# Performance work log

Measured on AMD Instinct MI355X. Metric: run time of the kernel, lower is better.

## Reference

```python
import jax, jax.numpy as jnp
import numpy as np
import math

D_MODEL = 1024
EXPAND = 2
D_INNER = D_MODEL * EXPAND  # 2048
D_STATE = 16
DT_RANK = max(1, (D_MODEL + 15) // 16)  # 64
K = 4  # conv kernel size
B, S = 2, 2048


def silu(v):
    return v * jax.nn.sigmoid(v)


def setup_inputs() -> dict:
    key = jax.random.key(0)
    ks = jax.random.split(key, 12)
    sc = lambda fan_in: 1.0 / math.sqrt(fan_in)
    x = jax.random.normal(ks[0], (B, S, D_MODEL), dtype=jnp.float32)
    Win = jax.random.normal(ks[1], (D_MODEL, 2 * D_INNER), dtype=jnp.float32) * sc(D_MODEL)
    Wconv = jax.random.normal(ks[2], (D_INNER, 1, K), dtype=jnp.float32) * sc(K)
    bconv = jax.random.normal(ks[3], (D_INNER,), dtype=jnp.float32) * 0.01
    Wx = jax.random.normal(ks[4], (D_INNER, DT_RANK + 2 * D_STATE), dtype=jnp.float32) * sc(D_INNER)
    Wdt = jax.random.normal(ks[5], (DT_RANK, D_INNER), dtype=jnp.float32) * sc(DT_RANK)
    # dt_proj bias init: inverse-softplus of dt ~ LogUniform[1e-3, 1e-1]
    dt = jnp.exp(jax.random.uniform(ks[6], (D_INNER,)) * (math.log(0.1) - math.log(0.001)) + math.log(0.001))
    dt = jnp.clip(dt, 0.0001, None)
    bdt = dt + jnp.log(-jnp.expm1(-dt))
    a = jnp.arange(1, D_STATE + 1, dtype=jnp.float32)[None, :].repeat(D_INNER, axis=0)
    a = a + jax.random.uniform(ks[7], a.shape) * 0.1
    A_log = jnp.log(a)
    Dp = jnp.ones((D_INNER,), dtype=jnp.float32)
    Wout = jax.random.normal(ks[8], (D_INNER, D_MODEL), dtype=jnp.float32) * sc(D_INNER)
    return {"x": x, "Win": Win, "Wconv": Wconv, "bconv": bconv, "Wx": Wx,
            "Wdt": Wdt, "bdt": bdt, "A_log": A_log, "Dp": Dp, "Wout": Wout}


def causal_dw_conv(x, Wconv, bconv):
    # x: [B, S, C] -> depthwise causal conv along S
    xc = jnp.transpose(x, (0, 2, 1))  # [B, C, S]
    y = jax.lax.conv_general_dilated(
        xc, Wconv, window_strides=(1,), padding=[(K - 1, 0)],
        feature_group_count=D_INNER,
        dimension_numbers=("NCH", "OIH", "NCH"))
    y = y + bconv[None, :, None]
    return jnp.transpose(y, (0, 2, 1))  # [B, S, C]


def selective_scan(u, delta, b_term, c_term, A_log, Dp):
    # u, delta: [B,S,Di]; b_term, c_term: [B,S,Ds]
    a = -jnp.exp(A_log)  # [Di, Ds]
    delta_a = jnp.exp(delta[..., None] * a[None, None])            # [B,S,Di,Ds] fp32
    delta_b_u = (delta * u)[..., None] * b_term[:, :, None, :]     # [B,S,Di,Ds]
    du = u * Dp[None, None, :]                                     # [B,S,Di]
    # time-major for scan
    dA = jnp.transpose(delta_a, (1, 0, 2, 3))
    dBu = jnp.transpose(delta_b_u, (1, 0, 2, 3))
    c_t = jnp.transpose(c_term, (1, 0, 2))
    du_t = jnp.transpose(du, (1, 0, 2))

    def step(state, inp):
        dA_t, dBu_t, c, duv = inp
        state = dA_t * state + dBu_t                  # [B,Di,Ds]
        y = jnp.einsum("bdn,bn->bd", state, c) + duv  # [B,Di]
        return state, y

    init = jnp.zeros((u.shape[0], D_INNER, D_STATE), dtype=jnp.float32)
    _, ys = jax.lax.scan(step, init, (dA, dBu, c_t, du_t))
    return jnp.transpose(ys, (1, 0, 2))  # [B,S,Di]


def reference(x, Win, Wconv, bconv, Wx, Wdt, bdt, A_log, Dp, Wout):
    xz = x @ Win                              # [B,S,2*Di]
    x_branch, z_branch = jnp.split(xz, 2, axis=-1)
    x_branch = silu(causal_dw_conv(x_branch, Wconv, bconv))
    params = x_branch @ Wx                    # [B,S,R+2*Ds]
    delta, b_term, c_term = jnp.split(params, [DT_RANK, DT_RANK + D_STATE], axis=-1)
    delta = jax.nn.softplus(delta @ Wdt + bdt)
    y = selective_scan(x_branch, delta, b_term, c_term, A_log, Dp)
    y = y * silu(z_branch)
    return y @ Wout
```

## Files before the change

### kernel.cpp

```cpp
#include <hip/hip_runtime.h>

typedef unsigned short u16;
typedef _Float16 f16;
typedef f16 f16x8 __attribute__((ext_vector_type(8)));
typedef u16 u16x8 __attribute__((ext_vector_type(8)));
typedef short s16x8 __attribute__((ext_vector_type(8)));
typedef float f32x4 __attribute__((ext_vector_type(4)));
typedef float f32x8 __attribute__((ext_vector_type(8)));

#define T_TOK 4096
#define B_SZ 2
#define S_LEN 2048
#define DMODEL 1024
#define DI 2048
#define DS 16
#define RNK 64
#define NCH 64
#define CLEN 32
#define LDXZ 4096
#define SK 8
#define PRM_SLICE (4096 * 128)
#define LOG2E 1.4426950408889634f

#define GLOAD_LDS16(gp, lp)                                                                   \
  __builtin_amdgcn_global_load_lds((const __attribute__((address_space(1))) void*)(gp),       \
                                   (__attribute__((address_space(3))) void*)(lp), 16, 0, 0)

__device__ __forceinline__ float b2f(u16 v) { return __uint_as_float(((unsigned)v) << 16); }
__device__ __forceinline__ u16 f2b(float f) {
  unsigned u = __float_as_uint(f);
  return (u16)((u + 0x7fffu + ((u >> 16) & 1u)) >> 16);
}
__device__ __forceinline__ float fexp2(float x) {
#if __has_builtin(__builtin_amdgcn_exp2f)
  return __builtin_amdgcn_exp2f(x);
#else
  return exp2f(x);
#endif
}
__device__ __forceinline__ int dtype_of(const void* dp) {
  unsigned v = *(const unsigned*)dp;
  return (v == 0x3F800000u) ? 0 : (v == 0x3C003C00u) ? 2 : 1;
}
__device__ __forceinline__ float load_any(const void* p, size_t i, int flag) {
  if (flag == 0) return ((const float*)p)[i];
  if (flag == 1) return b2f(((const u16*)p)[i]);
  return (float)((const f16*)p)[i];
}

__device__ __forceinline__ void tr_tile(const void* __restrict__ src, void* __restrict__ dst,
                                        int R, int C, int Cpad, int f, int bx, int by, int ob) {
  __shared__ f16 t[32][33];
  int c0 = bx * 32, r0 = by * 32;
  int tx = threadIdx.x & 31, ty = threadIdx.x >> 5;
#pragma unroll
  for (int i = ty; i < 32; i += 8) {
    int r = r0 + i, c = c0 + tx;
    float v = (r < R && c < C) ? load_any(src, (size_t)r * C + c, f) : 0.f;
    t[i][tx] = (f16)v;
  }
  __syncthreads();
#pragma unroll
  for (int i = ty; i < 32; i += 8) {
    int c = c0 + i, r = r0 + tx;
    if (c < Cpad && r < R) {
      if (ob) ((u16*)dst)[(size_t)c * R + r] = f2b((float)t[tx][i]);
      else ((f16*)dst)[(size_t)c * R + r] = t[tx][i];
    }
  }
}

__global__ __launch_bounds__(256) void k_prep(const void* __restrict__ Wconv, const void* __restrict__ bconv,
                                              const void* __restrict__ bdt, const void* __restrict__ A_log,
                                              const void* __restrict__ Dp, const void* __restrict__ Wx,
                                              const void* __restrict__ Wdt, const void* __restrict__ Win,
                                              const void* __restrict__ x, f16* __restrict__ WxT,
                                              f16* __restrict__ WdtT, u16* __restrict__ WinTb,
                                              u16* __restrict__ xhb, float* __restrict__ a_f,
                                              float* __restrict__ wconv_f, float* __restrict__ bconv_f,
                                              float* __restrict__ bdt_f, float* __restrict__ dp_f,
                                              int* __restrict__ flag) {
  int f = dtype_of(Dp);
  int bid = blockIdx.x, t = threadIdx.x;
  if (bid < 128) {
    int i = bid * 256 + t;
    a_f[i] = -__expf(load_any(A_log, i, f)) * LOG2E;
  } else if (bid < 160) {
    int i = (bid - 128) * 256 + t;
    wconv_f[i] = load_any(Wconv, i, f);
  } else if (bid < 168) {
    int i = (bid - 160) * 256 + t;
    bconv_f[i] = load_any(bconv, i, f);
  } else if (bid < 176) {
    int i = (bid - 168) * 256 + t;
    bdt_f[i] = load_any(bdt, i, f);
  } else if (bid < 184) {
    int i = (bid - 176) * 256 + t;
    dp_f[i] = load_any(Dp, i, f);
  } else if (bid == 184) {
    if (t == 0) *flag = f;
  } else if (bid < 441) {
    int id = bid - 185;
    tr_tile(Wx, WxT, 2048, 96, 128, f, id & 3, id >> 2, 0);
  } else if (bid < 569) {
    int id = bid - 441;
    tr_tile(Wdt, WdtT, 64, 2048, 2048, f, id & 63, id >> 6, 0);
  } else if (bid < 4665) {
    int id = bid - 569;
    tr_tile(Win, WinTb, 1024, 4096, 4096, f, id & 127, id >> 7, 1);
  } else {
    if (f == 1) return;
    size_t i = (size_t)(bid - 4665) * 2048 + (size_t)t * 8;
    u16x8 o;
    if (f == 0) {
      const float* s = (const float*)x + i;
#pragma unroll
      for (int j = 0; j < 8; ++j) o[j] = f2b(s[j]);
    } else {
      const f16* s = (const f16*)x + i;
#pragma unroll
      for (int j = 0; j < 8; ++j) o[j] = f2b((float)s[j]);
    }
    *(u16x8*)(xhb + i) = o;
  }
}

__global__ __launch_bounds__(256) void k_transpose16(const void* __restrict__ src, f16* __restrict__ dst,
                                                     int R, int C, int Cpad, const void* __restrict__ Dp) {
  tr_tile(src, dst, R, C, Cpad, dtype_of(Dp), blockIdx.x, blockIdx.y, 0);
}

__global__ __launch_bounds__(256) void k_gemm1(const void* __restrict__ x0, const u16* __restrict__ xhb,
                                               const u16* __restrict__ Bw, f16* __restrict__ C,
                                               const int* __restrict__ flag) {
  constexpr int BM = 128, BN = 128, WM = 64, WN = 64, FM = 4, FN = 4;
  const int lda = 1024, ldb = 1024, ldc = LDXZ, klen = 1024;
  __shared__ __align__(16) u16 As[2 * BM * 32];
  __shared__ __align__(16) u16 Bs[2 * BN * 32];
  const u16* A = (*flag == 1) ? (const u16*)x0 : xhb;
  const int tid = threadIdx.x;
  const int wv = tid >> 6, ln = tid & 63;
  const int quad = ln >> 4, l16 = ln & 15;
  const int lrow = ln >> 2, lch = (ln & 3) * 8;
  const int m0 = blockIdx.y * BM, n0 = blockIdx.x * BN;
  const int wm = (wv & 1) * WM, wn = (wv >> 1) * WN;
  f32x4 acc[FM][FN] = {};
  for (int k0 = 0; k0 < klen; k0 += 64) {
    __syncthreads();
#pragma unroll
    for (int h = 0; h < 2; ++h) {
#pragma unroll
      for (int i = 0; i < BM / 64; ++i) {
        int r0 = wv * (BM / 4) + i * 16;
        GLOAD_LDS16(A + (size_t)(m0 + r0 + lrow) * lda + k0 + h * 32 + lch, As + h * BM * 32 + r0 * 32);
      }
#pragma unroll
      for (int i = 0; i < BN / 64; ++i) {
        int r0 = wv * (BN / 4) + i * 16;
        GLOAD_LDS16(Bw + (size_t)(n0 + r0 + lrow) * ldb + k0 + h * 32 + lch, Bs + h * BN * 32 + r0 * 32);
      }
    }
    __syncthreads();
#pragma unroll
    for (int h = 0; h < 2; ++h) {
      s16x8 af[FM], bf[FN];
#pragma unroll
      for (int i = 0; i < FM; ++i) af[i] = *(const s16x8*)(As + h * BM * 32 + (wm + i * 16 + l16) * 32 + quad * 8);
#pragma unroll
      for (int j = 0; j < FN; ++j) bf[j] = *(const s16x8*)(Bs + h * BN * 32 + (wn + j * 16 + l16) * 32 + quad * 8);
#pragma unroll
      for (int i = 0; i < FM; ++i)
#pragma unroll
        for (int j = 0; j < FN; ++j)
          acc[i][j] = __builtin_amdgcn_mfma_f32_16x16x32_bf16(af[i], bf[j], acc[i][j], 0, 0, 0);
    }
  }
#pragma unroll
  for (int i = 0; i < FM; ++i)
#pragma unroll
    for (int j = 0; j < FN; ++j)
#pragma unroll
      for (int r = 0; r < 4; ++r) {
        int row = m0 + wm + i * 16 + quad * 4 + r;
        int col = n0 + wn + j * 16 + l16;
        C[(size_t)row * ldc + col] = (f16)acc[i][j][r];
      }
}

template <int BM, int BN, int EPI>
__global__ __launch_bounds__(256) void k_gemm2(const f16* __restrict__ A, const f16* __restrict__ B,
                                               void* __restrict__ Cv, const float* __restrict__ bias,
                                               const int* __restrict__ flag,
                                               int klen, int lda, int ldb, int ldc) {
  constexpr int WM = BM / 2, WN = BN / 2;
  constexpr int FM = WM / 16, FN = WN / 16;
  __shared__ __align__(16) f16 As[2 * BM * 32];
  __shared__ __align__(16) f16 Bs[2 * BN * 32];
  const int tid = threadIdx.x;
  const int wv = tid >> 6, ln = tid & 63;
  const int quad = ln >> 4, l16 = ln & 15;
  const int lrow = ln >> 2, lch = (ln & 3) * 8;
  const int m0 = blockIdx.y * BM, n0 = blockIdx.x * BN;
  const int wm = (wv & 1) * WM, wn = (wv >> 1) * WN;
  const int kbase = blockIdx.z * klen;
  f32x4 acc[FM][FN] = {};
  for (int kk = 0; kk < klen; kk += 64) {
    const int k0 = kbase + kk;
    __syncthreads();
#pragma unroll
    for (int h = 0; h < 2; ++h) {
#pragma unroll
      for (int i = 0; i < BM / 64; ++i) {
        int r0 = wv * (BM / 4) + i * 16;
        GLOAD_LDS16(A + (size_t)(m0 + r0 + lrow) * lda + k0 + h * 32 + lch, As + h * BM * 32 + r0 * 32);
      }
#pragma unroll
      for (int i = 0; i < BN / 64; ++i) {
        int r0 = wv * (BN / 4) + i * 16;
        GLOAD_LDS16(B + (size_t)(n0 + r0 + lrow) * ldb + k0 + h * 32 + lch, Bs + h * BN * 32 + r0 * 32);
      }
    }
    __syncthreads();
#pragma unroll
    for (int h = 0; h < 2; ++h) {
      f16x8 af[FM], bf[FN];
#pragma unroll
      for (int i = 0; i < FM; ++i) af[i] = *(const f16x8*)(As + h * BM * 32 + (wm + i * 16 + l16) * 32 + quad * 8);
#pragma unroll
      for (int j = 0; j < FN; ++j) bf[j] = *(const f16x8*)(Bs + h * BN * 32 + (wn + j * 16 + l16) * 32 + quad * 8);
#pragma unroll
      for (int i = 0; i < FM; ++i)
#pragma unroll
        for (int j = 0; j < FN; ++j)
          acc[i][j] = __builtin_amdgcn_mfma_f32_16x16x32_f16(af[i], bf[j], acc[i][j], 0, 0, 0);
    }
  }
  int dflag = 1;
  if constexpr (EPI == 2) dflag = *flag;
  f16* Cz = (f16*)Cv;
  if constexpr (EPI == 4) Cz = (f16*)Cv + (size_t)blockIdx.z * PRM_SLICE;
#pragma unroll
  for (int i = 0; i < FM; ++i)
#pragma unroll
    for (int j = 0; j < FN; ++j)
#pragma unroll
      for (int r = 0; r < 4; ++r) {
        int row = m0 + wm + i * 16 + quad * 4 + r;
        int col = n0 + wn + j * 16 + l16;
        size_t ci = (size_t)row * ldc + col;
        float v = acc[i][j][r];
        if constexpr (EPI == 1) {
          v += bias[col];
          v = (v > 20.f) ? v : log1pf(__expf(v));
          Cz[ci] = (f16)v;
        } else if constexpr (EPI == 2) {
          if (dflag == 0) ((float*)Cv)[ci] = v;
          else if (dflag == 1) ((u16*)Cv)[ci] = f2b(v);
          else ((f16*)Cv)[ci] = (f16)v;
        } else {
          Cz[ci] = (f16)v;
        }
      }
}

__global__ __launch_bounds__(256) void k_sum_prm(const f16* __restrict__ parts, f16* __restrict__ prm,
                                                 float* __restrict__ prmBC) {
  size_t i = (size_t)(blockIdx.x * 256 + threadIdx.x) * 8;
  int col0 = (int)(i & 127);
  if (col0 >= 96) return;
  float s[8] = {};
#pragma unroll
  for (int z = 0; z < SK; ++z) {
    f16x8 v = *(const f16x8*)(parts + (size_t)z * PRM_SLICE + i);
#pragma unroll
    for (int j = 0; j < 8; ++j) s[j] += (float)v[j];
  }
  if (col0 < 64) {
    f16x8 o;
#pragma unroll
    for (int j = 0; j < 8; ++j) o[j] = (f16)s[j];
    *(f16x8*)(prm + i) = o;
  } else {
    size_t tok = i >> 7;
    f32x8 of;
#pragma unroll
    for (int j = 0; j < 8; ++j) of[j] = s[j];
    *(f32x8*)(prmBC + tok * 32 + (col0 - 64)) = of;
  }
}

__global__ __launch_bounds__(256) void k_conv_silu(const f16* __restrict__ xz, const float* __restrict__ Wconv,
                                                   const float* __restrict__ bconv, f16* __restrict__ xc) {
  int t = blockIdx.x;
  int s = t & (S_LEN - 1);
  int d8 = threadIdx.x * 8;
  float w[4][8];
#pragma unroll
  for (int i = 0; i < 8; ++i)
#pragma unroll
    for (int j = 0; j < 4; ++j) w[j][i] = Wconv[(d8 + i) * 4 + j];
  float acc[8];
#pragma unroll
  for (int i = 0; i < 8; ++i) acc[i] = bconv[d8 + i];
#pragma unroll
  for (int j = 0; j < 4; ++j) {
    int sl = s - 3 + j;
    if (sl >= 0) {
      f16x8 xv = *(const f16x8*)(xz + (size_t)(t - 3 + j) * LDXZ + d8);
#pragma unroll
      for (int i = 0; i < 8; ++i) acc[i] = fmaf((float)xv[i], w[j][i], acc[i]);
    }
  }
  f16x8 o;
#pragma unroll
  for (int i = 0; i < 8; ++i) {
    float v = acc[i];
    o[i] = (f16)(v / (1.f + __expf(-v)));
  }
  *(f16x8*)(xc + (size_t)t * DI + d8) = o;
}

__global__ __launch_bounds__(256) void k_scan_passA(const f16* __restrict__ dlt, const f16* __restrict__ u,
                                                    const float* __restrict__ prmBC, const float* __restrict__ a_f,
                                                    f16* __restrict__ lcs, float* __restrict__ sumdv) {
  int g = blockIdx.x * 256 + threadIdx.x;
  int nh = g & 1, p = g >> 1;
  int d = p & (DI - 1);
  int c = (p >> 11) & (NCH - 1);
  int b = p >> 17;
  f32x4 a0 = *(const f32x4*)(a_f + d * DS + nh * 8);
  f32x4 a1 = *(const f32x4*)(a_f + d * DS + nh * 8 + 4);
  float a[8] = {a0[0], a0[1], a0[2], a0[3], a1[0], a1[1], a1[2], a1[3]};
  float st[8] = {};
  float sumd = 0.f;
  int t0 = b * S_LEN + c * CLEN;
  const f16* dp = dlt + (size_t)t0 * LDXZ + d;
  const f16* up = u + (size_t)t0 * DI + d;
  const float* bp = prmBC + (size_t)t0 * 32 + nh * 8;
  float dl = (float)dp[0];
  float uv = (float)up[0];
  for (int s = 0; s < CLEN; ++s) {
    int sn = (s + 1 < CLEN) ? s + 1 : s;
    float dl_n = (float)dp[(size_t)sn * LDXZ];
    float uv_n = (float)up[(size_t)sn * DI];
    f32x8 bv = *(const f32x8*)(bp + (size_t)s * 32);
    sumd += dl;
    float dbu = dl * uv;
#pragma unroll
    for (int j = 0; j < 8; ++j) {
      float e = fexp2(dl * a[j]);
      st[j] = fmaf(e, st[j], dbu * bv[j]);
    }
    dl = dl_n;
    uv = uv_n;
  }
  f16x8 o;
#pragma unroll
  for (int j = 0; j < 8; ++j) o[j] = (f16)st[j];
  *(f16x8*)(lcs + (size_t)p * DS + nh * 8) = o;
  if (nh == 0) sumdv[p] = sumd;
}

__global__ __launch_bounds__(256) void k_scan_passB(f16* __restrict__ lcs, const float* __restrict__ sumdv,
                                                    const float* __restrict__ a_f) {
  int g = blockIdx.x * 256 + threadIdx.x;
  int n = g & 15, d = (g >> 4) & (DI - 1), b = g >> 15;
  float an = a_f[d * DS + n];
  float init = 0.f;
  for (int c = 0; c < NCH; ++c) {
    int p = (b * NCH + c) * DI + d;
    size_t idx = (size_t)p * DS + n;
    float l = (float)lcs[idx];
    lcs[idx] = (f16)init;
    init = fexp2(sumdv[p] * an) * init + l;
  }
}

__global__ __launch_bounds__(256) void k_scan_passC(const f16* __restrict__ dlt, const f16* __restrict__ u,
                                                    const float* __restrict__ prmBC, const float* __restrict__ a_f,
                                                    const float* __restrict__ dp_f, const f16* __restrict__ lcs,
                                                    f16* __restrict__ xz) {
  int g = blockIdx.x * 256 + threadIdx.x;
  int nh = g & 1, p = g >> 1;
  int d = p & (DI - 1);
  int c = (p >> 11) & (NCH - 1);
  int b = p >> 17;
  f32x4 a0 = *(const f32x4*)(a_f + d * DS + nh * 8);
  f32x4 a1 = *(const f32x4*)(a_f + d * DS + nh * 8 + 4);
  float a[8] = {a0[0], a0[1], a0[2], a0[3], a1[0], a1[1], a1[2], a1[3]};
  float st[8];
  f16x8 iv = *(const f16x8*)(lcs + (size_t)p * DS + nh * 8);
#pragma unroll
  for (int j = 0; j < 8; ++j) st[j] = (float)iv[j];
  float dpv = dp_f[d];
  int t0 = b * S_LEN + c * CLEN;
  const f16* dp = dlt + (size_t)t0 * LDXZ + d;
  const f16* up = u + (size_t)t0 * DI + d;
  const float* bp = prmBC + (size_t)t0 * 32 + nh * 8;
  f16* zp = xz + (size_t)t0 * LDXZ + DI + d;
  float dl = (float)dp[0];
  float uv = (float)up[0];
  float z = (float)zp[0];
  for (int s = 0; s < CLEN; ++s) {
    int sn = (s + 1 < CLEN) ? s + 1 : s;
    float dl_n = (float)dp[(size_t)sn * LDXZ];
    float uv_n = (float)up[(size_t)sn * DI];
    float z_n = (float)zp[(size_t)sn * LDXZ];
    f32x8 bv = *(const f32x8*)(bp + (size_t)s * 32);
    f32x8 cv = *(const f32x8*)(bp + (size_t)s * 32 + 16);
    float dbu = dl * uv;
    float part = (nh == 0) ? uv * dpv : 0.f;
#pragma unroll
    for (int j = 0; j < 8; ++j) {
      float e = fexp2(dl * a[j]);
      st[j] = fmaf(e, st[j], dbu * bv[j]);
      part = fmaf(st[j], cv[j], part);
    }
    part += __shfl_xor(part, 1, 64);
    if (nh == 0) {
      float sg = 1.f / (1.f + __expf(-z));
      zp[(size_t)s * LDXZ] = (f16)(part * z * sg);
    }
    dl = dl_n;
    uv = uv_n;
    z = z_n;
  }
}

extern "C" void kernel_launch(void* const* d_in, const int* in_sizes, int n_in,
                              void* d_out, int out_size, void* d_ws, size_t ws_size,
                              hipStream_t stream) {
  const void* x = d_in[0];
  const void* Win = d_in[1];
  const void* Wconv = d_in[2];
  const void* bconv = d_in[3];
  const void* Wx = d_in[4];
  const void* Wdt = d_in[5];
  const void* bdt = d_in[6];
  const void* A_log = d_in[7];
  const void* Dp = d_in[8];
  const void* Wout = d_in[9];
  (void)in_sizes; (void)n_in; (void)out_size; (void)ws_size;

  const size_t KB = 1024, MB = 1024 * 1024;
  char* ws = (char*)d_ws;
  f16* xzh = (f16*)ws;
  u16* xhb = (u16*)(ws + 32 * MB);
  f16* xch = (f16*)(ws + 32 * MB);
  u16* WinTb = (u16*)(ws + 48 * MB);
  f16* parts = (f16*)(ws + 48 * MB);
  f16* lcs = (f16*)(ws + 48 * MB);
  f16* WoutT = (f16*)(ws + 48 * MB);
  float* sumd = (float*)(ws + 56 * MB);
  f16* prm = (f16*)(ws + 57 * MB);
  float* prmBC = (float*)(ws + 58 * MB);
  f16* WxT = (f16*)(ws + 58 * MB + 512 * KB);
  f16* WdtT = (f16*)(ws + 59 * MB);
  float* a_f = (float*)(ws + 59 * MB + 256 * KB);
  float* wconv_f = (float*)(ws + 59 * MB + 384 * KB);
  float* bconv_f = (float*)(ws + 59 * MB + 416 * KB);
  float* bdt_f = (float*)(ws + 59 * MB + 424 * KB);
  float* dp_f = (float*)(ws + 59 * MB + 432 * KB);
  int* flag = (int*)(ws + 59 * MB + 440 * KB);

  k_prep<<<6713, 256, 0, stream>>>(Wconv, bconv, bdt, A_log, Dp, Wx, Wdt, Win, x,
                                   WxT, WdtT, WinTb, xhb, a_f, wconv_f, bconv_f, bdt_f, dp_f, flag);

  k_gemm1<<<dim3(32, 32), 256, 0, stream>>>(x, xhb, WinTb, xzh, flag);
  k_conv_silu<<<T_TOK, 256, 0, stream>>>(xzh, wconv_f, bconv_f, xch);
  k_gemm2<64, 128, 4><<<dim3(1, 4096 / 64, SK), 256, 0, stream>>>(
      xch, WxT, parts, nullptr, flag, 2048 / SK, 2048, 2048, 128);
  k_sum_prm<<<PRM_SLICE / 8 / 256, 256, 0, stream>>>(parts, prm, prmBC);
  k_gemm2<128, 128, 1><<<dim3(2048 / 128, 4096 / 128), 256, 0, stream>>>(
      prm, WdtT, xzh, bdt_f, flag, 64, 128, 64, LDXZ);
  k_scan_passA<<<(B_SZ * NCH * DI * 2) / 256, 256, 0, stream>>>(xzh, xch, prmBC, a_f, lcs, sumd);
  k_scan_passB<<<(B_SZ * DI * DS) / 256, 256, 0, stream>>>(lcs, sumd, a_f);
  k_scan_passC<<<(B_SZ * NCH * DI * 2) / 256, 256, 0, stream>>>(xzh, xch, prmBC, a_f, dp_f, lcs, xzh);
  k_transpose16<<<dim3(1024 / 32, 2048 / 32), 256, 0, stream>>>(Wout, WoutT, 2048, 1024, 1024, Dp);
  k_gemm2<64, 128, 2><<<dim3(1024 / 128, 4096 / 64), 256, 0, stream>>>(
      xzh + DI, WoutT, d_out, nullptr, flag, 2048, LDXZ, 2048, 1024);
}
```

Before: 345.7 us.

## Rewrite input projection GEMM as 256x256 tile with pipelined swizzled LDS staging

Replaces the 128x128 tile, 4-wave in-projection GEMM with a 256x256 tile, 8-wave kernel. It double-buffers quarter tiles in LDS, issues global-to-LDS loads interleaved across eight compute phases with explicit vmcnt waits, and uses an XOR-swizzled LDS layout to avoid bank conflicts. MFMA priority is raised with setprio. The aim is to hide memory latency and raise data reuse per block. The trade-off is fewer blocks (256) on a large-CU part and 128KB of LDS per block, which limits occupancy.

```diff
diff --git a/kernel.cpp b/kernel.cpp
--- a/kernel.cpp
+++ b/kernel.cpp
@@ -130,60 +130,114 @@
   tr_tile(src, dst, R, C, Cpad, dtype_of(Dp), blockIdx.x, blockIdx.y, 0);
 }
 
-__global__ __launch_bounds__(256) void k_gemm1(const void* __restrict__ x0, const u16* __restrict__ xhb,
+__global__ __launch_bounds__(512) void k_gemm1(const void* __restrict__ x0, const u16* __restrict__ xhb,
                                                const u16* __restrict__ Bw, f16* __restrict__ C,
                                                const int* __restrict__ flag) {
-  constexpr int BM = 128, BN = 128, WM = 64, WN = 64, FM = 4, FN = 4;
-  const int lda = 1024, ldb = 1024, ldc = LDXZ, klen = 1024;
-  __shared__ __align__(16) u16 As[2 * BM * 32];
-  __shared__ __align__(16) u16 Bs[2 * BN * 32];
+  constexpr int LD = 1024, LDC = LDXZ, NT = 16, NP = NT / 2;
+  __shared__ __align__(16) u16 lds[8 * 8192];
   const u16* A = (*flag == 1) ? (const u16*)x0 : xhb;
   const int tid = threadIdx.x;
   const int wv = tid >> 6, ln = tid & 63;
   const int quad = ln >> 4, l16 = ln & 15;
-  const int lrow = ln >> 2, lch = (ln & 3) * 8;
-  const int m0 = blockIdx.y * BM, n0 = blockIdx.x * BN;
-  const int wm = (wv & 1) * WM, wn = (wv >> 1) * WN;
-  f32x4 acc[FM][FN] = {};
-  for (int k0 = 0; k0 < klen; k0 += 64) {
-    __syncthreads();
-#pragma unroll
-    for (int h = 0; h < 2; ++h) {
-#pragma unroll
-      for (int i = 0; i < BM / 64; ++i) {
-        int r0 = wv * (BM / 4) + i * 16;
-        GLOAD_LDS16(A + (size_t)(m0 + r0 + lrow) * lda + k0 + h * 32 + lch, As + h * BM * 32 + r0 * 32);
-      }
-#pragma unroll
-      for (int i = 0; i < BN / 64; ++i) {
-        int r0 = wv * (BN / 4) + i * 16;
-        GLOAD_LDS16(Bw + (size_t)(n0 + r0 + lrow) * ldb + k0 + h * 32 + lch, Bs + h * BN * 32 + r0 * 32);
-      }
-    }
-    __syncthreads();
-#pragma unroll
-    for (int h = 0; h < 2; ++h) {
-      s16x8 af[FM], bf[FN];
-#pragma unroll
-      for (int i = 0; i < FM; ++i) af[i] = *(const s16x8*)(As + h * BM * 32 + (wm + i * 16 + l16) * 32 + quad * 8);
-#pragma unroll
-      for (int j = 0; j < FN; ++j) bf[j] = *(const s16x8*)(Bs + h * BN * 32 + (wn + j * 16 + l16) * 32 + quad * 8);
-#pragma unroll
-      for (int i = 0; i < FM; ++i)
-#pragma unroll
-        for (int j = 0; j < FN; ++j)
-          acc[i][j] = __builtin_amdgcn_mfma_f32_16x16x32_bf16(af[i], bf[j], acc[i][j], 0, 0, 0);
-    }
-  }
-#pragma unroll
-  for (int i = 0; i < FM; ++i)
-#pragma unroll
-    for (int j = 0; j < FN; ++j)
+  const int wr = wv >> 2, wc = wv & 3;
+  const int m0 = blockIdx.y * 256, n0 = blockIdx.x * 256;
+  const int rr = tid >> 3;
+  const int cc = (tid & 7) ^ (rr & 7);
+  const u16* aBase = A + (size_t)m0 * LD + cc * 8;
+  const u16* bBase = Bw + (size_t)n0 * LD + cc * 8;
+  const int brow = ((tid >> 8) << 6) + (rr & 31);
+  u16* const dBase = lds + wv * 512;
+  auto stageA = [&](int tile, int mq) {
+    const u16* s = aBase + (size_t)(mq * 64 + rr) * LD + tile * 64;
+    u16* d = dBase + ((tile & 1) * 4 + mq) * 8192;
+    GLOAD_LDS16(s, d);
+    GLOAD_LDS16(s + 128 * LD, d + 4096);
+  };
+  auto stageB = [&](int tile, int nq) {
+    const u16* s = bBase + (size_t)(brow + nq * 32) * LD + tile * 64;
+    u16* d = dBase + ((tile & 1) * 4 + 2 + nq) * 8192;
+    GLOAD_LDS16(s, d);
+    GLOAD_LDS16(s + 128 * LD, d + 4096);
+  };
+  const int rxor = (l16 & 7) << 3;
+  f32x4 acc[8][4] = {};
+  stageA(0, 0); stageB(0, 1); stageB(0, 0); stageA(0, 1);
+  stageA(1, 0); stageB(1, 1);
+  asm volatile("s_waitcnt vmcnt(4)" ::: "memory");
+  __builtin_amdgcn_s_barrier();
+  s16x8 af[4][2], bf[2][2];
+  for (int pr = 0; pr < NP; ++pr) {
+    const int t0 = 2 * pr;
+    const bool more = (pr < NP - 1);
+#pragma unroll
+    for (int ph = 0; ph < 8; ++ph) {
+      const int slot = ph >> 2, q = ph & 3;
+      const int mq = q >> 1, nq = (q >> 1) ^ (q & 1);
+      const u16* Ar = lds + (slot * 4 + mq) * 8192;
+      const u16* Br = lds + (slot * 4 + 2 + nq) * 8192;
+      if (q == 0 || q == 2) {
+#pragma unroll
+        for (int i = 0; i < 4; ++i) {
+          const int ra = wr * 64 + i * 16 + l16;
+#pragma unroll
+          for (int kk = 0; kk < 2; ++kk)
+            af[i][kk] = *(const s16x8*)(Ar + ra * 64 + ((kk * 32 + quad * 8) ^ rxor));
+        }
+      }
+      if (q != 2) {
+#pragma unroll
+        for (int j = 0; j < 2; ++j) {
+          const int rb = wc * 32 + j * 16 + l16;
+#pragma unroll
+          for (int kk = 0; kk < 2; ++kk)
+            bf[j][kk] = *(const s16x8*)(Br + rb * 64 + ((kk * 32 + quad * 8) ^ rxor));
+        }
+      }
+      if (ph == 0) stageB(t0 + 1, 0);
+      else if (ph == 1) stageA(t0 + 1, 1);
+      else if (more) {
+        if (ph == 2) stageA(t0 + 2, 0);
+        else if (ph == 3) stageB(t0 + 2, 1);
+        else if (ph == 4) stageB(t0 + 2, 0);
+        else if (ph == 5) stageA(t0 + 2, 1);
+        else if (ph == 6) stageA(t0 + 3, 0);
+        else stageB(t0 + 3, 1);
+      }
+      __builtin_amdgcn_s_barrier();
+      asm volatile("s_waitcnt lgkmcnt(0)" ::: "memory");
+      __builtin_amdgcn_sched_barrier(0);
+      __builtin_amdgcn_s_setprio(1);
+#pragma unroll
+      for (int kk = 0; kk < 2; ++kk)
+#pragma unroll
+        for (int i = 0; i < 4; ++i)
+#pragma unroll
+          for (int j = 0; j < 2; ++j)
+            acc[mq * 4 + i][nq * 2 + j] = __builtin_amdgcn_mfma_f32_16x16x32_bf16(
+                af[i][kk], bf[j][kk], acc[mq * 4 + i][nq * 2 + j], 0, 0, 0);
+      __builtin_amdgcn_s_setprio(0);
+      if (ph == 3) {
+        if (more) asm volatile("s_waitcnt vmcnt(6)" ::: "memory");
+        else asm volatile("s_waitcnt vmcnt(2)" ::: "memory");
+      } else if (ph == 5) {
+        if (more) asm volatile("s_waitcnt vmcnt(8)" ::: "memory");
+        else asm volatile("s_waitcnt vmcnt(0)" ::: "memory");
+      } else if (ph == 7) {
+        if (more) asm volatile("s_waitcnt vmcnt(4)" ::: "memory");
+        else asm volatile("s_waitcnt vmcnt(0)" ::: "memory");
+      }
+      __builtin_amdgcn_s_barrier();
+    }
+  }
+#pragma unroll
+  for (int i = 0; i < 8; ++i)
+#pragma unroll
+    for (int j = 0; j < 4; ++j)
 #pragma unroll
       for (int r = 0; r < 4; ++r) {
-        int row = m0 + wm + i * 16 + quad * 4 + r;
-        int col = n0 + wn + j * 16 + l16;
-        C[(size_t)row * ldc + col] = (f16)acc[i][j][r];
+        const int row = m0 + wr * 128 + i * 16 + quad * 4 + r;
+        const int col = n0 + wc * 64 + j * 16 + l16;
+        C[(size_t)row * LDC + col] = (f16)acc[i][j][r];
       }
 }
 
@@ -466,7 +520,7 @@
   k_prep<<<6713, 256, 0, stream>>>(Wconv, bconv, bdt, A_log, Dp, Wx, Wdt, Win, x,
                                    WxT, WdtT, WinTb, xhb, a_f, wconv_f, bconv_f, bdt_f, dp_f, flag);
 
-  k_gemm1<<<dim3(32, 32), 256, 0, stream>>>(x, xhb, WinTb, xzh, flag);
+  k_gemm1<<<dim3(16, 16), 512, 0, stream>>>(x, xhb, WinTb, xzh, flag);
   k_conv_silu<<<T_TOK, 256, 0, stream>>>(xzh, wconv_f, bconv_f, xch);
   k_gemm2<64, 128, 4><<<dim3(1, 4096 / 64, SK), 256, 0, stream>>>(
       xch, WxT, parts, nullptr, flag, 2048 / SK, 2048, 2048, 128);
```

After: 334.3 us. 1.03x faster.
